# Optimization experiments

Measured on AMD Instinct MI355X. Metric: run time of the kernel, lower is better.

The kernel has to match this reference:

```python
import jax, jax.numpy as jnp
import numpy as np

B, A, N, T = 4, 66000, 30, 5          # batch, anchors, max gt boxes, max label tags
NUM_CLASSES = [10, 23, 69, 163, 12]    # agents, actions, duplexes, triplets, locations
C_TOTAL = 1 + sum(NUM_CLASSES)         # 278 (first channel is binary objectness)
ALPHA, GAMMA, BETA = 0.25, 2.0, 1.0 / 9.0


def setup_inputs() -> dict:
    key = jax.random.key(0)
    ks = jax.random.split(key, 5)
    confidence = jax.random.normal(ks[0], (B, A, C_TOTAL), jnp.float32)
    predicted_locations = jax.random.normal(ks[1], (B, A, 4), jnp.float32)
    gt_locations = jax.random.normal(ks[2], (B, A, 4), jnp.float32)
    # per-task label tags in [-1, numc); -1 means 'no more tags' (break in one_hot_labels)
    gt_labels = jnp.stack(
        [jax.random.randint(jax.random.fold_in(ks[3], i), (B, N, T), -1, NUM_CLASSES[i])
         for i in range(len(NUM_CLASSES))], axis=2).astype(jnp.int32)  # [B, N, 5, T]
    # matched anchor state: -1 ignore, 0 background, n>0 -> gt box n-1
    labels_bin = (jax.random.randint(ks[4], (B, A), 0, N + 2) - 1).astype(jnp.int32)
    return {"confidence": confidence, "predicted_locations": predicted_locations,
            "gt_locations": gt_locations, "gt_labels": gt_labels, "labels_bin": labels_bin}


def _focal_elem(logits, labels):
    # BCE(sigmoid(x), y) in numerically-stable logits form, then focal weighting
    bce = jnp.maximum(logits, 0.0) - logits * labels + jnp.log1p(jnp.exp(-jnp.abs(logits)))
    p = jax.nn.sigmoid(logits)
    pt = p * labels + (1.0 - p) * (1.0 - labels)
    alpha_factor = ALPHA * labels + (1.0 - ALPHA) * (1.0 - labels)
    return bce * alpha_factor * (1.0 - pt) ** GAMMA


def reference(confidence, predicted_locations, gt_locations, gt_labels, labels_bin):
    dtype = confidence.dtype
    dumy = jnp.maximum(labels_bin, 0)                       # [B,A] gather index (ignore->bg)
    mask = (labels_bin > -1).astype(dtype)                   # [B,A] not-ignored
    pos = (labels_bin > 0).astype(dtype)                     # [B,A] positives
    num_pos = jnp.maximum(1.0, pos.sum())

    diff = jnp.abs(predicted_locations - gt_locations)       # [B,A,4]
    sl1 = jnp.where(diff < BETA, 0.5 * diff * diff / BETA, diff - 0.5 * BETA)
    regression_loss = (sl1 * pos[..., None]).sum() / (num_pos * 4.0)

    # binary (objectness) focal loss on channel 0
    cls_loss = (_focal_elem(confidence[:, :, 0], pos) * mask).sum() / num_pos

    cc = 1
    for nlt, nc in enumerate(NUM_CLASSES):
        tgt = gt_labels[:, :, nlt, :]                        # [B,N,T]
        # one_hot_labels: stop at first negative tag (break semantics)
        valid = jnp.cumprod((tgt >= 0).astype(jnp.int32), axis=-1).astype(dtype)  # [B,N,T]
        oh = jax.nn.one_hot(jnp.clip(tgt, 0, nc - 1), nc, dtype=dtype) * valid[..., None]
        table = jnp.minimum(oh.sum(axis=2), 1.0)             # [B,N,nc] per-gt multi-hot
        table = jnp.concatenate([jnp.zeros((B, 1, nc), dtype), table], axis=1)  # bg row 0
        labels = jnp.take_along_axis(table, dumy[:, :, None], axis=1)           # [B,A,nc]
        logits = confidence[:, :, cc:cc + nc]                # [B,A,nc]
        cls_loss = cls_loss + (_focal_elem(logits, labels) * mask[..., None]).sum() / num_pos
        cc += nc
    return (regression_loss, cls_loss)
```

## Files before the change

### kernel.cpp

```cpp
#include <hip/hip_runtime.h>

#define B_    4
#define A_    66000
#define NA_   (B_ * A_)
#define N_    30
#define T_    5
#define NLT   5
#define CSUM  277
#define CTOT  278
#define ROWS  31
#define NROWS (B_ * ROWS)
#define WPR   11
#define NBW   (NROWS * WPR)
#define NE    (NA_ * CTOT)
#define NE16  (NE / 16)

#define BLK       256
#define GRID_CLS  2048
#define GRID_PREP 512

typedef float fx4 __attribute__((ext_vector_type(4)));
typedef float fx2 __attribute__((ext_vector_type(2)));


__device__ __forceinline__ fx2 pair_focal(float x0, float x1, unsigned b2,
                                          float c25, float c75, fx2 acc) {
    bool y0 = (b2 & 1u) != 0u, y1 = (b2 & 2u) != 0u;
    float s0 = y0 ? -x0 : x0,  s1 = y1 ? -x1 : x1;
    float k0 = y0 ? c25 : c75, k1 = y1 ? c25 : c75;
    float t0 = __builtin_amdgcn_exp2f(-fabsf(x0) * 1.4426950408889634f);
    float t1 = __builtin_amdgcn_exp2f(-fabsf(x1) * 1.4426950408889634f);
    fx2 t = {t0, t1};
    fx2 u = t + 1.0f;
    fx2 L = { __builtin_amdgcn_logf(u.x), __builtin_amdgcn_logf(u.y) };
    fx2 sp = { fmaxf(s0, 0.f), fmaxf(s1, 0.f) };
    sp += L * 0.6931471805599453f;
    fx2 inv = { __builtin_amdgcn_rcpf(u.x), __builtin_amdgcn_rcpf(u.y) };
    fx2 ti = t * inv;
    fx2 sig = { s0 >= 0.f ? inv.x : ti.x, s1 >= 0.f ? inv.y : ti.y };
    fx2 term = { k0, k1 };
    term *= sp;
    return acc + term * (sig * sig);
}

__device__ __forceinline__ float sl1(float d) {
    float ad = fabsf(d);
    return (ad < (1.f / 9.f)) ? 4.5f * ad * ad : ad - (1.f / 18.f);
}

__device__ __forceinline__ float block_reduce(float v, float* sdata) {
    #pragma unroll
    for (int off = 32; off > 0; off >>= 1) v += __shfl_down(v, off, 64);
    int lane = threadIdx.x & 63, wid = threadIdx.x >> 6;
    if (lane == 0) sdata[wid] = v;
    __syncthreads();
    int nw = blockDim.x >> 6;
    if (wid == 0) {
        v = (lane < nw) ? sdata[lane] : 0.f;
        #pragma unroll
        for (int off = 32; off > 0; off >>= 1) v += __shfl_down(v, off, 64);
    }
    return v;
}


__global__ __launch_bounds__(BLK) void prep_kernel(
    const int* __restrict__ gtl, const int* __restrict__ lbin,
    const float* __restrict__ pred, const float* __restrict__ gt,
    unsigned* __restrict__ bits, int* __restrict__ rowid,
    float* __restrict__ reg_part, float* __restrict__ pos_part)
{
    if (blockIdx.x == 0) {
        for (int i = threadIdx.x; i < NBW; i += BLK) bits[i] = 0u;
        __syncthreads();
        int tid = threadIdx.x;
        if (tid < NROWS && (tid % ROWS) > 0) atomicOr(&bits[tid * WPR], 1u);
        for (int idx = tid; idx < B_ * N_ * NLT; idx += BLK) {
            int lt = idx % NLT;
            int bn = idx / NLT;
            int n  = bn % N_;
            int b  = bn / N_;
            const int nc_arr[NLT]  = {10, 23, 69, 163, 12};
            const int off_arr[NLT] = {0, 10, 33, 102, 265};
            int nc  = nc_arr[lt];
            int off = off_arr[lt] + 1;
            const int* g = gtl + (size_t)(((b * N_ + n) * NLT + lt)) * T_;
            int row = b * ROWS + (n + 1);
            bool valid = true;
            #pragma unroll
            for (int t = 0; t < T_; ++t) {
                int v = g[t];
                valid = valid && (v >= 0);
                if (valid) {
                    int c = off + ((v < nc) ? v : (nc - 1));
                    atomicOr(&bits[row * WPR + (c >> 5)], 1u << (c & 31));
                }
            }
        }
        if (tid == 0) rowid[NA_] = 0;
    }

    float racc = 0.f, pacc = 0.f;
    unsigned stride = gridDim.x * BLK;
    for (unsigned i = blockIdx.x * BLK + threadIdx.x; i < NA_; i += stride) {
        int lb = lbin[i];
        unsigned b = i / A_;
        rowid[i] = (lb < 0) ? -1 : (int)((b * ROWS + (unsigned)(lb > 0 ? lb : 0)) * WPR);
        if (lb > 0) {
            pacc += 1.f;
            float4 pv = *(const float4*)(pred + (size_t)4 * i);
            float4 gv = *(const float4*)(gt + (size_t)4 * i);
            racc += sl1(pv.x - gv.x) + sl1(pv.y - gv.y) + sl1(pv.z - gv.z) + sl1(pv.w - gv.w);
        }
    }
    __shared__ float sdata[BLK / 64];
    float r = block_reduce(racc, sdata);
    __syncthreads();
    float p = block_reduce(pacc, sdata);
    if (threadIdx.x == 0) {
        reg_part[blockIdx.x] = r;
        pos_part[blockIdx.x] = p;
    }
}

__global__ __launch_bounds__(BLK) void cls_kernel(
    const fx4* __restrict__ conf4, const int* __restrict__ rowid,
    const unsigned* __restrict__ bits, float* __restrict__ partials)
{
    __shared__ unsigned lbits[NBW];
    for (int i = threadIdx.x; i < NBW; i += BLK) lbits[i] = bits[i];
    __syncthreads();

    fx2 acc2 = {0.f, 0.f};
    unsigned stride = gridDim.x * BLK;
    for (unsigned i = blockIdx.x * BLK + threadIdx.x; i < NE16; i += stride) {
        fx4 x0 = conf4[4u * i];
        fx4 x1 = conf4[4u * i + 1u];
        fx4 x2 = conf4[4u * i + 2u];
        fx4 x3 = conf4[4u * i + 3u];
        unsigned i16 = i * 16u;
        unsigned a  = i16 / CTOT;
        unsigned c0 = i16 - a * CTOT;
        int ridA = rowid[a];
        int ridB = rowid[a + 1u];
        unsigned bwA = (ridA >= 0) ? (unsigned)ridA : 0u;
        unsigned bwB = (ridB >= 0) ? (unsigned)ridB : 0u;
        float mA = (ridA >= 0) ? 1.f : 0.f;
        float mB = (ridB >= 0) ? 1.f : 0.f;
        float c25A = 0.25f * mA, c75A = 0.75f * mA;
        float c25B = 0.25f * mB, c75B = 0.75f * mB;
        unsigned wi = c0 >> 5, sh = c0 & 31u;
        unsigned w0  = lbits[bwA + wi];
        unsigned w1  = lbits[bwA + wi + 1u];
        unsigned wB0 = lbits[bwB];
        unsigned wfull = (unsigned)((((unsigned long long)w1 << 32) | w0) >> sh);
        unsigned bnd  = CTOT - c0;
        bool cross    = bnd < 16u;
        unsigned w16  = cross ? ((wfull & ((1u << bnd) - 1u)) | (wB0 << bnd))
                              : wfull;
        #define PSEL(k) ((cross && bnd <= (2u*(k))) )
        float q25_1 = PSEL(1) ? c25B : c25A, q75_1 = PSEL(1) ? c75B : c75A;
        float q25_2 = PSEL(2) ? c25B : c25A, q75_2 = PSEL(2) ? c75B : c75A;
        float q25_3 = PSEL(3) ? c25B : c25A, q75_3 = PSEL(3) ? c75B : c75A;
        float q25_4 = PSEL(4) ? c25B : c25A, q75_4 = PSEL(4) ? c75B : c75A;
        float q25_5 = PSEL(5) ? c25B : c25A, q75_5 = PSEL(5) ? c75B : c75A;
        float q25_6 = PSEL(6) ? c25B : c25A, q75_6 = PSEL(6) ? c75B : c75A;
        float q25_7 = PSEL(7) ? c25B : c25A, q75_7 = PSEL(7) ? c75B : c75A;
        #undef PSEL
        acc2 = pair_focal(x0.x, x0.y,  w16 & 3u,        c25A, c75A, acc2);
        acc2 = pair_focal(x0.z, x0.w, (w16 >>  2) & 3u, q25_1, q75_1, acc2);
        acc2 = pair_focal(x1.x, x1.y, (w16 >>  4) & 3u, q25_2, q75_2, acc2);
        acc2 = pair_focal(x1.z, x1.w, (w16 >>  6) & 3u, q25_3, q75_3, acc2);
        acc2 = pair_focal(x2.x, x2.y, (w16 >>  8) & 3u, q25_4, q75_4, acc2);
        acc2 = pair_focal(x2.z, x2.w, (w16 >> 10) & 3u, q25_5, q75_5, acc2);
        acc2 = pair_focal(x3.x, x3.y, (w16 >> 12) & 3u, q25_6, q75_6, acc2);
        acc2 = pair_focal(x3.z, x3.w, (w16 >> 14) & 3u, q25_7, q75_7, acc2);
    }

    __shared__ float sdata[BLK / 64];
    float r = block_reduce(acc2.x + acc2.y, sdata);
    if (threadIdx.x == 0) partials[blockIdx.x] = r;
}

__global__ void finalize_kernel(
    const float* __restrict__ cls_part, const float* __restrict__ reg_part,
    const float* __restrict__ pos_part, float* __restrict__ out)
{
    __shared__ float sdata[256 / 64];
    float c = 0.f, r = 0.f, pz = 0.f;
    for (int i = threadIdx.x; i < GRID_CLS; i += blockDim.x) c += cls_part[i];
    for (int i = threadIdx.x; i < GRID_PREP; i += blockDim.x) {
        r  += reg_part[i];
        pz += pos_part[i];
    }
    c = block_reduce(c, sdata);
    __syncthreads();
    r = block_reduce(r, sdata);
    __syncthreads();
    pz = block_reduce(pz, sdata);
    if (threadIdx.x == 0) {
        float np = fmaxf(1.f, pz);
        out[0] = r / (np * 4.f);
        out[1] = c / np;
    }
}


extern "C" void kernel_launch(void* const* d_in, const int* in_sizes, int n_in,
                              void* d_out, int out_size, void* d_ws, size_t ws_size,
                              hipStream_t stream) {
    const float* conf = (const float*)d_in[0];
    const float* pred = (const float*)d_in[1];
    const float* gt   = (const float*)d_in[2];
    const int*   gtl  = (const int*)d_in[3];
    const int*   lbin = (const int*)d_in[4];
    float* out = (float*)d_out;

    unsigned* bits  = (unsigned*)d_ws;
    int* rowid      = (int*)(bits + NBW);
    float* cls_part = (float*)(rowid + NA_ + 1);
    float* reg_part = cls_part + GRID_CLS;
    float* pos_part = reg_part + GRID_PREP;

    hipLaunchKernelGGL(prep_kernel, dim3(GRID_PREP), dim3(BLK), 0, stream,
                       gtl, lbin, pred, gt, bits, rowid, reg_part, pos_part);
    hipLaunchKernelGGL(cls_kernel, dim3(GRID_CLS), dim3(BLK), 0, stream,
                       (const fx4*)conf, rowid, bits, cls_part);
    hipLaunchKernelGGL(finalize_kernel, dim3(1), dim3(256), 0, stream,
                       cls_part, reg_part, pos_part, out);
}
```

Baseline: 73.20 us.

## Fuse prep kernel into classification kernel, building label bit table per block

Removes the separate prep kernel. Each classification block now builds the per-gt multi-hot bit table directly in shared memory, and the smooth-L1 and positive-count partials are computed inside the same kernel. The main loop reads labels_bin directly instead of a precomputed rowid array, which drops one launch and the global rowid/bits write-then-read round trip. In exchange, every one of the 2048 blocks redundantly reads gt_labels and performs shared-memory atomics before its main loop, adding per-block setup latency.

After: 67.26 us. 8.1% less time.

```diff
diff --git a/kernel.cpp b/kernel.cpp
--- a/kernel.cpp
+++ b/kernel.cpp
@@ -17,7 +17,6 @@
 
 #define BLK       256
 #define GRID_CLS  2048
-#define GRID_PREP 512
 
 typedef float fx4 __attribute__((ext_vector_type(4)));
 typedef float fx2 __attribute__((ext_vector_type(2)));
@@ -64,72 +63,56 @@
 }
 
 
-__global__ __launch_bounds__(BLK) void prep_kernel(
-    const int* __restrict__ gtl, const int* __restrict__ lbin,
+__global__ __launch_bounds__(BLK) void cls_kernel(
+    const fx4* __restrict__ conf4, const int* __restrict__ lbin,
+    const int* __restrict__ gtl,
     const float* __restrict__ pred, const float* __restrict__ gt,
-    unsigned* __restrict__ bits, int* __restrict__ rowid,
-    float* __restrict__ reg_part, float* __restrict__ pos_part)
+    float* __restrict__ cls_part, float* __restrict__ reg_part,
+    float* __restrict__ pos_part)
 {
-    if (blockIdx.x == 0) {
-        for (int i = threadIdx.x; i < NBW; i += BLK) bits[i] = 0u;
-        __syncthreads();
-        int tid = threadIdx.x;
-        if (tid < NROWS && (tid % ROWS) > 0) atomicOr(&bits[tid * WPR], 1u);
-        for (int idx = tid; idx < B_ * N_ * NLT; idx += BLK) {
-            int lt = idx % NLT;
-            int bn = idx / NLT;
-            int n  = bn % N_;
-            int b  = bn / N_;
-            const int nc_arr[NLT]  = {10, 23, 69, 163, 12};
-            const int off_arr[NLT] = {0, 10, 33, 102, 265};
-            int nc  = nc_arr[lt];
-            int off = off_arr[lt] + 1;
-            const int* g = gtl + (size_t)(((b * N_ + n) * NLT + lt)) * T_;
-            int row = b * ROWS + (n + 1);
-            bool valid = true;
-            #pragma unroll
-            for (int t = 0; t < T_; ++t) {
-                int v = g[t];
-                valid = valid && (v >= 0);
-                if (valid) {
-                    int c = off + ((v < nc) ? v : (nc - 1));
-                    atomicOr(&bits[row * WPR + (c >> 5)], 1u << (c & 31));
-                }
+    __shared__ unsigned lbits[NBW];
+    for (int i = threadIdx.x; i < NBW; i += BLK) lbits[i] = 0u;
+    __syncthreads();
+    for (int r = threadIdx.x; r < NROWS; r += BLK)
+        if ((r % ROWS) != 0) atomicOr(&lbits[r * WPR], 1u);
+    for (int idx = threadIdx.x; idx < B_ * N_ * NLT; idx += BLK) {
+        int lt = idx % NLT;
+        int bn = idx / NLT;
+        int n  = bn % N_;
+        int b  = bn / N_;
+        const int nc_arr[NLT]  = {10, 23, 69, 163, 12};
+        const int off_arr[NLT] = {0, 10, 33, 102, 265};
+        int nc  = nc_arr[lt];
+        int off = off_arr[lt] + 1;
+        const int* g = gtl + (size_t)(((b * N_ + n) * NLT + lt)) * T_;
+        int row = b * ROWS + (n + 1);
+        bool valid = true;
+        #pragma unroll
+        for (int t = 0; t < T_; ++t) {
+            int v = g[t];
+            valid = valid && (v >= 0);
+            if (valid) {
+                int c = off + ((v < nc) ? v : (nc - 1));
+                atomicOr(&lbits[row * WPR + (c >> 5)], 1u << (c & 31));
             }
         }
-        if (tid == 0) rowid[NA_] = 0;
-    }
+    }
+    __syncthreads();
 
     float racc = 0.f, pacc = 0.f;
-    unsigned stride = gridDim.x * BLK;
-    for (unsigned i = blockIdx.x * BLK + threadIdx.x; i < NA_; i += stride) {
-        int lb = lbin[i];
-        unsigned b = i / A_;
-        rowid[i] = (lb < 0) ? -1 : (int)((b * ROWS + (unsigned)(lb > 0 ? lb : 0)) * WPR);
-        if (lb > 0) {
-            pacc += 1.f;
-            float4 pv = *(const float4*)(pred + (size_t)4 * i);
-            float4 gv = *(const float4*)(gt + (size_t)4 * i);
-            racc += sl1(pv.x - gv.x) + sl1(pv.y - gv.y) + sl1(pv.z - gv.z) + sl1(pv.w - gv.w);
+    {
+        unsigned i = blockIdx.x * BLK + threadIdx.x;
+        if (i < NA_) {
+            int lb = lbin[i];
+            if (lb > 0) {
+                pacc = 1.f;
+                float4 pv = *(const float4*)(pred + (size_t)4 * i);
+                float4 gv = *(const float4*)(gt + (size_t)4 * i);
+                racc = sl1(pv.x - gv.x) + sl1(pv.y - gv.y)
+                     + sl1(pv.z - gv.z) + sl1(pv.w - gv.w);
+            }
         }
     }
-    __shared__ float sdata[BLK / 64];
-    float r = block_reduce(racc, sdata);
-    __syncthreads();
-    float p = block_reduce(pacc, sdata);
-    if (threadIdx.x == 0) {
-        reg_part[blockIdx.x] = r;
-        pos_part[blockIdx.x] = p;
-    }
-}
-
-__global__ __launch_bounds__(BLK) void cls_kernel(
-    const fx4* __restrict__ conf4, const int* __restrict__ rowid,
-    const unsigned* __restrict__ bits, float* __restrict__ partials)
-{
-    __shared__ unsigned lbits[NBW];
-    for (int i = threadIdx.x; i < NBW; i += BLK) lbits[i] = bits[i];
-    __syncthreads();
 
     fx2 acc2 = {0.f, 0.f};
     unsigned stride = gridDim.x * BLK;
@@ -141,12 +124,18 @@
         unsigned i16 = i * 16u;
         unsigned a  = i16 / CTOT;
         unsigned c0 = i16 - a * CTOT;
-        int ridA = rowid[a];
-        int ridB = rowid[a + 1u];
-        unsigned bwA = (ridA >= 0) ? (unsigned)ridA : 0u;
-        unsigned bwB = (ridB >= 0) ? (unsigned)ridB : 0u;
-        float mA = (ridA >= 0) ? 1.f : 0.f;
-        float mB = (ridB >= 0) ? 1.f : 0.f;
+        unsigned bA = a / A_;
+        unsigned rA = a - bA * A_;
+        unsigned bB = bA + ((rA + 1u == A_) ? 1u : 0u);
+        int lbA = lbin[a];
+        int lbB = lbin[(a + 1u < NA_) ? (a + 1u) : (NA_ - 1u)];
+        bool okA = lbA >= 0, okB = lbB >= 0;
+        unsigned duA = (lbA > 0) ? (unsigned)lbA : 0u;
+        unsigned duB = (lbB > 0) ? (unsigned)lbB : 0u;
+        unsigned bwA = okA ? (bA * ROWS + duA) * WPR : 0u;
+        unsigned bwB = okB ? (bB * ROWS + duB) * WPR : 0u;
+        float mA = okA ? 1.f : 0.f;
+        float mB = okB ? 1.f : 0.f;
         float c25A = 0.25f * mA, c75A = 0.75f * mA;
         float c25B = 0.25f * mB, c75B = 0.75f * mB;
         unsigned wi = c0 >> 5, sh = c0 & 31u;
@@ -178,8 +167,16 @@
     }
 
     __shared__ float sdata[BLK / 64];
-    float r = block_reduce(acc2.x + acc2.y, sdata);
-    if (threadIdx.x == 0) partials[blockIdx.x] = r;
+    float rc = block_reduce(acc2.x + acc2.y, sdata);
+    __syncthreads();
+    float rr = block_reduce(racc, sdata);
+    __syncthreads();
+    float rp = block_reduce(pacc, sdata);
+    if (threadIdx.x == 0) {
+        cls_part[blockIdx.x] = rc;
+        reg_part[blockIdx.x] = rr;
+        pos_part[blockIdx.x] = rp;
+    }
 }
 
 __global__ void finalize_kernel(
@@ -188,8 +185,8 @@
 {
     __shared__ float sdata[256 / 64];
     float c = 0.f, r = 0.f, pz = 0.f;
-    for (int i = threadIdx.x; i < GRID_CLS; i += blockDim.x) c += cls_part[i];
-    for (int i = threadIdx.x; i < GRID_PREP; i += blockDim.x) {
+    for (int i = threadIdx.x; i < GRID_CLS; i += blockDim.x) {
+        c  += cls_part[i];
         r  += reg_part[i];
         pz += pos_part[i];
     }
@@ -216,16 +213,13 @@
     const int*   lbin = (const int*)d_in[4];
     float* out = (float*)d_out;
 
-    unsigned* bits  = (unsigned*)d_ws;
-    int* rowid      = (int*)(bits + NBW);
-    float* cls_part = (float*)(rowid + NA_ + 1);
+    float* cls_part = (float*)d_ws;
     float* reg_part = cls_part + GRID_CLS;
-    float* pos_part = reg_part + GRID_PREP;
-
-    hipLaunchKernelGGL(prep_kernel, dim3(GRID_PREP), dim3(BLK), 0, stream,
-                       gtl, lbin, pred, gt, bits, rowid, reg_part, pos_part);
+    float* pos_part = reg_part + GRID_CLS;
+
     hipLaunchKernelGGL(cls_kernel, dim3(GRID_CLS), dim3(BLK), 0, stream,
-                       (const fx4*)conf, rowid, bits, cls_part);
+                       (const fx4*)conf, lbin, gtl, pred, gt,
+                       cls_part, reg_part, pos_part);
     hipLaunchKernelGGL(finalize_kernel, dim3(1), dim3(256), 0, stream,
                        cls_part, reg_part, pos_part, out);
 }
```
